# Kernel tuning notes

Measured on AMD Instinct MI355X. Metric: run time of the kernel, lower is better.

Reference implementation:

```python
import jax, jax.numpy as jnp
import numpy as np

N = 100000   # nodes
E = 800000   # directed edges (before self-loops)
D = 256      # in_feats == out_feats


def setup_inputs() -> dict:
    key = jax.random.key(0)
    ks = jax.random.split(key, 6)
    scale = 1.0 / np.sqrt(D)
    features = jax.random.normal(ks[0], (N, D), dtype=jnp.float32)
    src = jax.random.randint(ks[1], (E,), 0, N, dtype=jnp.int32)
    dst = jax.random.randint(ks[2], (E,), 0, N, dtype=jnp.int32)
    W1 = jax.random.normal(ks[3], (D, D), dtype=jnp.float32) * scale
    b1 = jnp.zeros((D,), dtype=jnp.float32)
    W2 = jax.random.normal(ks[4], (D, D), dtype=jnp.float32) * scale
    b2 = jnp.zeros((D,), dtype=jnp.float32)
    return {"features": features, "src": src, "dst": dst,
            "W1": W1, "b1": b1, "W2": W2, "b2": b2}


def _graph_conv(h, src, dst, norm_src, norm_dst, W, b):
    # DGL GraphConv, norm='both': out = D_in^{-1/2} A (D_out^{-1/2} h W) + b
    h = (h * norm_src) @ W            # [N, D] project (W first; in==out)
    agg = jax.ops.segment_sum(h[src], dst, num_segments=N)  # SpMM gather-scatter
    return agg * norm_dst + b


def reference(features, src, dst, W1, b1, W2, b2):
    # forward does g = dgl.add_self_loop(g)
    loops = jnp.arange(N, dtype=src.dtype)
    s = jnp.concatenate([src, loops])
    d = jnp.concatenate([dst, loops])
    ones = jnp.ones_like(s, dtype=jnp.float32)
    deg_out = jax.ops.segment_sum(ones, s, num_segments=N)   # out-degree (src side)
    deg_in = jax.ops.segment_sum(ones, d, num_segments=N)    # in-degree  (dst side)
    norm_src = jnp.where(deg_out > 0, deg_out ** -0.5, 0.0)[:, None]
    norm_dst = jnp.where(deg_in > 0, deg_in ** -0.5, 0.0)[:, None]
    x = _graph_conv(features, s, d, norm_src, norm_dst, W1, b1)
    x = jax.nn.relu(x)
    x = _graph_conv(x, s, d, norm_src, norm_dst, W2, b2)
    return x
```

## Files before the change

### kernel.cpp

```cpp
#include <hip/hip_runtime.h>

#define NN 100000
#define DD 256
#define SCAN_BLK 1024

typedef unsigned int uint;
typedef unsigned short ushort;
typedef __attribute__((ext_vector_type(8))) short bfx8;
typedef __attribute__((ext_vector_type(4))) float fx4;

__device__ __forceinline__ ushort f2bf(float f) {
    uint u = __float_as_uint(f);
    u += 0x7fff + ((u >> 16) & 1);
    return (ushort)(u >> 16);
}

__global__ __launch_bounds__(256) void k_init_deg(int* __restrict__ dego,
                                                  int* __restrict__ degi) {
    int i = blockIdx.x * 256 + threadIdx.x;
    if (i < NN) { dego[i] = 1; degi[i] = 1; }
}

__global__ __launch_bounds__(256) void k_count(const int* __restrict__ src,
                                               const int* __restrict__ dst, int E,
                                               int* __restrict__ dego,
                                               int* __restrict__ degi) {
    int e = blockIdx.x * 256 + threadIdx.x;
    if (e < E) {
        atomicAdd(&dego[src[e]], 1);
        atomicAdd(&degi[dst[e]], 1);
    }
}

__global__ __launch_bounds__(256) void k_norm(const int* __restrict__ dego,
                                              const int* __restrict__ degi,
                                              float* __restrict__ ns,
                                              float* __restrict__ nd) {
    int i = blockIdx.x * 256 + threadIdx.x;
    if (i < NN) {
        ns[i] = rsqrtf((float)dego[i]);
        nd[i] = rsqrtf((float)degi[i]);
    }
}

__device__ __forceinline__ int block_scan_inc(int v, int* sm) {
    int t = threadIdx.x;
    sm[t] = v;
    __syncthreads();
    for (int o = 1; o < SCAN_BLK; o <<= 1) {
        int x = (t >= o) ? sm[t - o] : 0;
        __syncthreads();
        sm[t] += x;
        __syncthreads();
    }
    return sm[t];
}

__global__ __launch_bounds__(SCAN_BLK) void k_scan1(const int* __restrict__ degi,
                                                    int* __restrict__ partials) {
    __shared__ int sm[SCAN_BLK];
    int i = blockIdx.x * SCAN_BLK + threadIdx.x;
    int v = (i < NN) ? (degi[i] - 1) : 0;
    block_scan_inc(v, sm);
    if (threadIdx.x == 0) partials[blockIdx.x] = sm[SCAN_BLK - 1];
}

__global__ __launch_bounds__(128) void k_scan2(int* __restrict__ partials, int nb) {
    __shared__ int sm[128];
    int t = threadIdx.x;
    int v = (t < nb) ? partials[t] : 0;
    sm[t] = v;
    __syncthreads();
    for (int o = 1; o < 128; o <<= 1) {
        int x = (t >= o) ? sm[t - o] : 0;
        __syncthreads();
        sm[t] += x;
        __syncthreads();
    }
    if (t < nb) partials[t] = sm[t] - v;
}

__global__ __launch_bounds__(SCAN_BLK) void k_scan3(const int* __restrict__ degi,
                                                    const int* __restrict__ partials,
                                                    int* __restrict__ rowptr,
                                                    int* __restrict__ cursor) {
    __shared__ int sm[SCAN_BLK];
    int i = blockIdx.x * SCAN_BLK + threadIdx.x;
    int v = (i < NN) ? (degi[i] - 1) : 0;
    int incl = block_scan_inc(v, sm);
    int excl = partials[blockIdx.x] + incl - v;
    if (i <= NN) rowptr[i] = excl;
    if (i < NN) cursor[i] = excl;
}

__global__ __launch_bounds__(256) void k_fill(const int* __restrict__ src,
                                              const int* __restrict__ dst, int E,
                                              int* __restrict__ cursor,
                                              int* __restrict__ eidx) {
    int e = blockIdx.x * 256 + threadIdx.x;
    if (e < E) {
        int d = dst[e];
        int p = atomicAdd(&cursor[d], 1);
        eidx[p] = src[e];
    }
}

__global__ __launch_bounds__(256) void k_convW(const float* __restrict__ W,
                                               ushort* __restrict__ Wt) {
    int n = blockIdx.x, k = threadIdx.x;
    Wt[n * DD + k] = f2bf(W[(size_t)k * DD + n]);
}

template <bool FP32A>
__global__ __launch_bounds__(512) void k_mfgemm(const void* __restrict__ Av,
                                                const float* __restrict__ nrm,
                                                const ushort* __restrict__ Wt,
                                                ushort* __restrict__ H) {
    __shared__ uint4 atq[2][256 * 8];
    __shared__ uint4 wtq[128 * 32];
    int t = threadIdx.x;
    int brow = blockIdx.x * 256;
    int bcol = blockIdx.y * 128;
    int lane = t & 63, w = t >> 6;
    int wr = w >> 1, wc = w & 1;
    int lg = lane >> 4, lr = lane & 15;

    {
        const uint4* srcp = (const uint4*)Wt + (size_t)bcol * 32;
#pragma unroll
        for (int i = 0; i < 8; ++i) {
            int q = i * 512 + t;
            int n = q >> 5, c = q & 31;
            wtq[n * 32 + (c ^ (n & 7))] = srcp[q];
        }
    }

    int sr0 = t >> 3, sc0 = t & 7;
    int rows_[4];
    float ns_[4];
#pragma unroll
    for (int i = 0; i < 4; ++i) {
        int r = brow + sr0 + i * 64;
        if (r >= NN) r = NN - 1;
        rows_[i] = r;
        if (FP32A) ns_[i] = nrm[r];
    }

    fx4 acc[4][4];
#pragma unroll
    for (int mi = 0; mi < 4; ++mi)
#pragma unroll
        for (int ni = 0; ni < 4; ++ni)
            acc[mi][ni] = (fx4){0.f, 0.f, 0.f, 0.f};

    uint4 sv[4];
    float4 svf[4][2];

    auto ldA = [&](int ks) {
        if (FP32A) {
            const float* X = (const float*)Av;
#pragma unroll
            for (int i = 0; i < 4; ++i) {
                const float4* p =
                    (const float4*)(X + (size_t)rows_[i] * DD + ks * 64 + sc0 * 8);
                svf[i][0] = p[0];
                svf[i][1] = p[1];
            }
        } else {
            const ushort* A = (const ushort*)Av;
#pragma unroll
            for (int i = 0; i < 4; ++i)
                sv[i] = *(const uint4*)(A + (size_t)rows_[i] * DD + ks * 64 + sc0 * 8);
        }
    };
    auto wrA = [&](int buf) {
#pragma unroll
        for (int i = 0; i < 4; ++i) {
            int r = sr0 + i * 64;
            uint4 u;
            if (FP32A) {
                float s = ns_[i];
                float4 a = svf[i][0], b = svf[i][1];
                u.x = (uint)f2bf(a.x * s) | ((uint)f2bf(a.y * s) << 16);
                u.y = (uint)f2bf(a.z * s) | ((uint)f2bf(a.w * s) << 16);
                u.z = (uint)f2bf(b.x * s) | ((uint)f2bf(b.y * s) << 16);
                u.w = (uint)f2bf(b.z * s) | ((uint)f2bf(b.w * s) << 16);
            } else {
                u = sv[i];
            }
            atq[buf][r * 8 + (sc0 ^ (r & 7))] = u;
        }
    };

    ldA(0);
    wrA(0);
    __syncthreads();

    int buf = 0;
    for (int ks = 0; ks < 4; ++ks) {
        if (ks < 3) ldA(ks + 1);
#pragma unroll
        for (int kk = 0; kk < 2; ++kk) {
            bfx8 af[4], bfr[4];
#pragma unroll
            for (int mi = 0; mi < 4; ++mi) {
                int r = wr * 64 + mi * 16 + lr;
                int c = kk * 4 + lg;
                af[mi] = *(const bfx8*)&atq[buf][r * 8 + (c ^ (r & 7))];
            }
#pragma unroll
            for (int ni = 0; ni < 4; ++ni) {
                int n = wc * 64 + ni * 16 + lr;
                int c2 = ks * 8 + kk * 4 + lg;
                bfr[ni] = *(const bfx8*)&wtq[n * 32 + (c2 ^ (n & 7))];
            }
#pragma unroll
            for (int mi = 0; mi < 4; ++mi)
#pragma unroll
                for (int ni = 0; ni < 4; ++ni)
                    acc[mi][ni] = __builtin_amdgcn_mfma_f32_16x16x32_bf16(
                        af[mi], bfr[ni], acc[mi][ni], 0, 0, 0);
        }
        if (ks < 3) wrA(buf ^ 1);
        __syncthreads();
        buf ^= 1;
    }

#pragma unroll
    for (int mi = 0; mi < 4; ++mi) {
        int rbase = brow + wr * 64 + mi * 16 + lg * 4;
#pragma unroll
        for (int ni = 0; ni < 4; ++ni) {
            int col = bcol + wc * 64 + ni * 16 + lr;
#pragma unroll
            for (int j = 0; j < 4; ++j) {
                int row = rbase + j;
                if (row < NN) H[(size_t)row * DD + col] = f2bf(acc[mi][ni][j]);
            }
        }
    }
}

__global__ __launch_bounds__(256) void k_spmm_bf(const ushort* __restrict__ T,
                                                 const int* __restrict__ rowptr,
                                                 const int* __restrict__ eidx,
                                                 const float* __restrict__ nd,
                                                 const float* __restrict__ ns,
                                                 const float* __restrict__ bias,
                                                 ushort* __restrict__ obf,
                                                 float* __restrict__ of,
                                                 int layer1) {
    int wid = threadIdx.x >> 6, lane = threadIdx.x & 63;
    int node = blockIdx.x * 4 + wid;
    if (node >= NN) return;
    int c = lane << 2;
    uint2 sv = *(const uint2*)(T + (size_t)node * DD + c);
    float p0[4], p1[4], p2[4], p3[4];
    p0[0] = __uint_as_float(sv.x << 16);
    p0[1] = __uint_as_float(sv.x & 0xffff0000u);
    p0[2] = __uint_as_float(sv.y << 16);
    p0[3] = __uint_as_float(sv.y & 0xffff0000u);
#pragma unroll
    for (int j = 0; j < 4; ++j) { p1[j] = 0.f; p2[j] = 0.f; p3[j] = 0.f; }
    int e = rowptr[node], end = rowptr[node + 1];
    for (; e + 3 < end; e += 4) {
        int s0 = eidx[e], s1 = eidx[e + 1], s2 = eidx[e + 2], s3 = eidx[e + 3];
        uint2 v0 = *(const uint2*)(T + (size_t)s0 * DD + c);
        uint2 v1 = *(const uint2*)(T + (size_t)s1 * DD + c);
        uint2 v2 = *(const uint2*)(T + (size_t)s2 * DD + c);
        uint2 v3 = *(const uint2*)(T + (size_t)s3 * DD + c);
        p0[0] += __uint_as_float(v0.x << 16);
        p0[1] += __uint_as_float(v0.x & 0xffff0000u);
        p0[2] += __uint_as_float(v0.y << 16);
        p0[3] += __uint_as_float(v0.y & 0xffff0000u);
        p1[0] += __uint_as_float(v1.x << 16);
        p1[1] += __uint_as_float(v1.x & 0xffff0000u);
        p1[2] += __uint_as_float(v1.y << 16);
        p1[3] += __uint_as_float(v1.y & 0xffff0000u);
        p2[0] += __uint_as_float(v2.x << 16);
        p2[1] += __uint_as_float(v2.x & 0xffff0000u);
        p2[2] += __uint_as_float(v2.y << 16);
        p2[3] += __uint_as_float(v2.y & 0xffff0000u);
        p3[0] += __uint_as_float(v3.x << 16);
        p3[1] += __uint_as_float(v3.x & 0xffff0000u);
        p3[2] += __uint_as_float(v3.y << 16);
        p3[3] += __uint_as_float(v3.y & 0xffff0000u);
    }
    for (; e < end; ++e) {
        int s0 = eidx[e];
        uint2 v0 = *(const uint2*)(T + (size_t)s0 * DD + c);
        p0[0] += __uint_as_float(v0.x << 16);
        p0[1] += __uint_as_float(v0.x & 0xffff0000u);
        p0[2] += __uint_as_float(v0.y << 16);
        p0[3] += __uint_as_float(v0.y & 0xffff0000u);
    }
#pragma unroll
    for (int j = 0; j < 4; ++j) p0[j] += (p1[j] + p2[j]) + p3[j];
    float n = nd[node];
    float4 bb = *(const float4*)(bias + c);
    float o0 = fmaf(p0[0], n, bb.x);
    float o1 = fmaf(p0[1], n, bb.y);
    float o2 = fmaf(p0[2], n, bb.z);
    float o3 = fmaf(p0[3], n, bb.w);
    if (layer1) {
        float s = ns[node];
        o0 = fmaxf(o0, 0.f) * s; o1 = fmaxf(o1, 0.f) * s;
        o2 = fmaxf(o2, 0.f) * s; o3 = fmaxf(o3, 0.f) * s;
        uint lo = (uint)f2bf(o0) | ((uint)f2bf(o1) << 16);
        uint hi = (uint)f2bf(o2) | ((uint)f2bf(o3) << 16);
        *(uint2*)(obf + (size_t)node * DD + c) = make_uint2(lo, hi);
    } else {
        fx4 o = {o0, o1, o2, o3};
        __builtin_nontemporal_store(o, (fx4*)(of + (size_t)node * DD + c));
    }
}

extern "C" void kernel_launch(void* const* d_in, const int* in_sizes, int n_in,
                              void* d_out, int out_size, void* d_ws, size_t ws_size,
                              hipStream_t stream) {
    const float* features = (const float*)d_in[0];
    const int* src = (const int*)d_in[1];
    const int* dst = (const int*)d_in[2];
    const float* W1 = (const float*)d_in[3];
    const float* b1 = (const float*)d_in[4];
    const float* W2 = (const float*)d_in[5];
    const float* b2 = (const float*)d_in[6];
    int E = in_sizes[1];
    float* out = (float*)d_out;

    size_t off = 0;
    auto alloc = [&](size_t nbytes) -> void* {
        void* p = (char*)d_ws + off;
        off += (nbytes + 255) & ~(size_t)255;
        return p;
    };
    int* dego = (int*)alloc((size_t)NN * 4);
    int* degi = (int*)alloc((size_t)NN * 4);
    float* norm_src = (float*)alloc((size_t)NN * 4);
    float* norm_dst = (float*)alloc((size_t)NN * 4);
    int* rowptr = (int*)alloc((size_t)(NN + 1) * 4);
    int* cursor = (int*)alloc((size_t)NN * 4);
    int* partials = (int*)alloc(128 * 4);
    int* eidx = (int*)alloc((size_t)E * 4);
    ushort* Wt1 = (ushort*)alloc((size_t)DD * DD * 2);
    ushort* Wt2 = (ushort*)alloc((size_t)DD * DD * 2);
    ushort* Xbf = (ushort*)alloc((size_t)NN * DD * 2);
    ushort* Hbf = (ushort*)alloc((size_t)NN * DD * 2);

    const int NB = (NN + SCAN_BLK - 1) / SCAN_BLK;

    k_init_deg<<<(NN + 255) / 256, 256, 0, stream>>>(dego, degi);
    k_count<<<(E + 255) / 256, 256, 0, stream>>>(src, dst, E, dego, degi);
    k_norm<<<(NN + 255) / 256, 256, 0, stream>>>(dego, degi, norm_src, norm_dst);
    k_scan1<<<NB, SCAN_BLK, 0, stream>>>(degi, partials);
    k_scan2<<<1, 128, 0, stream>>>(partials, NB);
    k_scan3<<<NB, SCAN_BLK, 0, stream>>>(degi, partials, rowptr, cursor);
    k_fill<<<(E + 255) / 256, 256, 0, stream>>>(src, dst, E, cursor, eidx);

    k_convW<<<DD, DD, 0, stream>>>(W1, Wt1);
    k_convW<<<DD, DD, 0, stream>>>(W2, Wt2);

    dim3 ggrid((NN + 255) / 256, 2);
    k_mfgemm<true><<<ggrid, 512, 0, stream>>>(features, norm_src, Wt1, Hbf);
    k_spmm_bf<<<(NN + 3) / 4, 256, 0, stream>>>(Hbf, rowptr, eidx, norm_dst,
                                                norm_src, b1, Xbf, out, 1);
    k_mfgemm<false><<<ggrid, 512, 0, stream>>>(Xbf, nullptr, Wt2, Hbf);
    k_spmm_bf<<<(NN + 3) / 4, 256, 0, stream>>>(Hbf, rowptr, eidx, norm_dst,
                                                norm_src, b2, nullptr, out, 0);
}
```

Before: 384.9 us.

## Retile GEMM to 128x256 blocks covering full output width, streaming W per k-step

The GEMM block tile changes from 256 rows by 128 columns (two column blocks) to 128 rows by the full 256 columns. Each A row is therefore read from global memory once instead of twice, which matters most for the fp32 feature input. W is now streamed in double-buffered 64-wide k-slices alongside A rather than preloaded whole for a column half. The trade-off is more W traffic per block and a different LDS footprint and per-wave layout.

```diff
diff --git a/kernel.cpp b/kernel.cpp
--- a/kernel.cpp
+++ b/kernel.cpp
@@ -116,31 +116,21 @@
                                                 const float* __restrict__ nrm,
                                                 const ushort* __restrict__ Wt,
                                                 ushort* __restrict__ H) {
-    __shared__ uint4 atq[2][256 * 8];
-    __shared__ uint4 wtq[128 * 32];
+    __shared__ uint4 atq[2][128 * 8];
+    __shared__ uint4 wtq[2][256 * 8];
     int t = threadIdx.x;
-    int brow = blockIdx.x * 256;
-    int bcol = blockIdx.y * 128;
+    int brow = blockIdx.x * 128;
     int lane = t & 63, w = t >> 6;
-    int wr = w >> 1, wc = w & 1;
+    int wr = w >> 2, wc = w & 3;
     int lg = lane >> 4, lr = lane & 15;
 
-    {
-        const uint4* srcp = (const uint4*)Wt + (size_t)bcol * 32;
-#pragma unroll
-        for (int i = 0; i < 8; ++i) {
-            int q = i * 512 + t;
-            int n = q >> 5, c = q & 31;
-            wtq[n * 32 + (c ^ (n & 7))] = srcp[q];
-        }
-    }
-
-    int sr0 = t >> 3, sc0 = t & 7;
-    int rows_[4];
-    float ns_[4];
-#pragma unroll
-    for (int i = 0; i < 4; ++i) {
-        int r = brow + sr0 + i * 64;
+    int sr = t >> 3, sc = t & 7;
+
+    int rows_[2];
+    float ns_[2];
+#pragma unroll
+    for (int i = 0; i < 2; ++i) {
+        int r = brow + sr + i * 64;
         if (r >= NN) r = NN - 1;
         rows_[i] = r;
         if (FP32A) ns_[i] = nrm[r];
@@ -153,30 +143,39 @@
         for (int ni = 0; ni < 4; ++ni)
             acc[mi][ni] = (fx4){0.f, 0.f, 0.f, 0.f};
 
-    uint4 sv[4];
-    float4 svf[4][2];
+    uint4 sva[2];
+    float4 svf[2][2];
+    uint4 svw[4];
 
     auto ldA = [&](int ks) {
         if (FP32A) {
             const float* X = (const float*)Av;
 #pragma unroll
-            for (int i = 0; i < 4; ++i) {
+            for (int i = 0; i < 2; ++i) {
                 const float4* p =
-                    (const float4*)(X + (size_t)rows_[i] * DD + ks * 64 + sc0 * 8);
+                    (const float4*)(X + (size_t)rows_[i] * DD + ks * 64 + sc * 8);
                 svf[i][0] = p[0];
                 svf[i][1] = p[1];
             }
         } else {
             const ushort* A = (const ushort*)Av;
 #pragma unroll
-            for (int i = 0; i < 4; ++i)
-                sv[i] = *(const uint4*)(A + (size_t)rows_[i] * DD + ks * 64 + sc0 * 8);
+            for (int i = 0; i < 2; ++i)
+                sva[i] = *(const uint4*)(A + (size_t)rows_[i] * DD + ks * 64 + sc * 8);
+        }
+    };
+    auto ldW = [&](int ks) {
+        const uint4* Wq = (const uint4*)Wt;
+#pragma unroll
+        for (int i = 0; i < 4; ++i) {
+            int n = sr + i * 64;
+            svw[i] = Wq[(size_t)n * 32 + ks * 8 + sc];
         }
     };
     auto wrA = [&](int buf) {
 #pragma unroll
-        for (int i = 0; i < 4; ++i) {
-            int r = sr0 + i * 64;
+        for (int i = 0; i < 2; ++i) {
+            int r = sr + i * 64;
             uint4 u;
             if (FP32A) {
                 float s = ns_[i];
@@ -186,19 +185,28 @@
                 u.z = (uint)f2bf(b.x * s) | ((uint)f2bf(b.y * s) << 16);
                 u.w = (uint)f2bf(b.z * s) | ((uint)f2bf(b.w * s) << 16);
             } else {
-                u = sv[i];
-            }
-            atq[buf][r * 8 + (sc0 ^ (r & 7))] = u;
+                u = sva[i];
+            }
+            atq[buf][r * 8 + (sc ^ (r & 7))] = u;
+        }
+    };
+    auto wrW = [&](int buf) {
+#pragma unroll
+        for (int i = 0; i < 4; ++i) {
+            int n = sr + i * 64;
+            wtq[buf][n * 8 + (sc ^ (n & 7))] = svw[i];
         }
     };
 
     ldA(0);
+    ldW(0);
     wrA(0);
+    wrW(0);
     __syncthreads();
 
     int buf = 0;
     for (int ks = 0; ks < 4; ++ks) {
-        if (ks < 3) ldA(ks + 1);
+        if (ks < 3) { ldA(ks + 1); ldW(ks + 1); }
 #pragma unroll
         for (int kk = 0; kk < 2; ++kk) {
             bfx8 af[4], bfr[4];
@@ -211,8 +219,8 @@
 #pragma unroll
             for (int ni = 0; ni < 4; ++ni) {
                 int n = wc * 64 + ni * 16 + lr;
-                int c2 = ks * 8 + kk * 4 + lg;
-                bfr[ni] = *(const bfx8*)&wtq[n * 32 + (c2 ^ (n & 7))];
+                int c2 = kk * 4 + lg;
+                bfr[ni] = *(const bfx8*)&wtq[buf][n * 8 + (c2 ^ (n & 7))];
             }
 #pragma unroll
             for (int mi = 0; mi < 4; ++mi)
@@ -221,7 +229,7 @@
                     acc[mi][ni] = __builtin_amdgcn_mfma_f32_16x16x32_bf16(
                         af[mi], bfr[ni], acc[mi][ni], 0, 0, 0);
         }
-        if (ks < 3) wrA(buf ^ 1);
+        if (ks < 3) { wrA(buf ^ 1); wrW(buf ^ 1); }
         __syncthreads();
         buf ^= 1;
     }
@@ -231,7 +239,7 @@
         int rbase = brow + wr * 64 + mi * 16 + lg * 4;
 #pragma unroll
         for (int ni = 0; ni < 4; ++ni) {
-            int col = bcol + wc * 64 + ni * 16 + lr;
+            int col = wc * 64 + ni * 16 + lr;
 #pragma unroll
             for (int j = 0; j < 4; ++j) {
                 int row = rbase + j;
@@ -360,7 +368,7 @@
     k_convW<<<DD, DD, 0, stream>>>(W1, Wt1);
     k_convW<<<DD, DD, 0, stream>>>(W2, Wt2);
 
-    dim3 ggrid((NN + 255) / 256, 2);
+    dim3 ggrid((NN + 127) / 128);
     k_mfgemm<true><<<ggrid, 512, 0, stream>>>(features, norm_src, Wt1, Hbf);
     k_spmm_bf<<<(NN + 3) / 4, 256, 0, stream>>>(Hbf, rowptr, eidx, norm_dst,
                                                 norm_src, b1, Xbf, out, 1);
```

After: 390.8 us. No clear change (+1.5%).
